# Performance work log

Hardware: AMD Instinct MI355X
Metric: run time of the kernel (lower is better)

The kernel has to match this reference:

```python
import jax, jax.numpy as jnp
import numpy as np

G = 16          # groups
K = 5           # kernel_size
IPG = 1024 // G # in_channels_per_group
OPG = 1024 // G # out_channels_per_group


def setup_inputs() -> dict:
    key = jax.random.key(0)
    k1, k2, k3 = jax.random.split(key, 3)
    inputs = jax.random.normal(k1, (4, 4096, 1024), dtype=jnp.float32)
    positions = jnp.sort(
        jax.random.randint(k2, (4, 4096), 0, 8192, dtype=jnp.int32), axis=-1)
    # kaiming-uniform-like init for kernel [G, OPG, IPG, K]
    fan_in = IPG * K
    bound = float(np.sqrt(6.0 / fan_in))
    kernel = jax.random.uniform(k3, (G, OPG, IPG, K), dtype=jnp.float32,
                                minval=-bound, maxval=bound)
    return {"inputs": inputs, "positions": positions, "kernel": kernel}


def reference(inputs, positions, kernel):
    B, L, C = inputs.shape
    c = K // 2
    # pad sequence dim; pad positions with -1 sentinel (never matches expected)
    pi = jnp.pad(inputs, ((0, 0), (c, c), (0, 0)))            # [B, L+2c, C]
    pp = jnp.pad(positions, ((0, 0), (c, c)), constant_values=-1)  # [B, L+2c]
    # sliding-window gather indices (equivalent to unfold with stride 1)
    idx = jnp.arange(L)[:, None] + jnp.arange(K)[None, :]      # [L, K]
    ip = pi[:, idx, :]        # [B, L, K, C] input patches
    ppatch = pp[:, idx]       # [B, L, K]  position patches
    # center of each patch is the original position at that output index
    offsets = jnp.arange(-c, c + 1, dtype=positions.dtype)    # [K]
    expected = positions[:, :, None] + offsets                # [B, L, K]
    mask = (ppatch == expected).astype(inputs.dtype)          # [B, L, K]
    masked = ip * mask[..., None]                             # [B, L, K, C]
    # split channels into groups: [B, L, K, G, IPG]
    gp = masked.reshape(B, L, K, G, IPG)
    # grouped conv reduce over in_channels_per_group and kernel taps
    out = jnp.einsum('blkgi,goik->blgo', gp, kernel)           # [B, L, G, OPG]
    return out
```

## Files before the change

kernel.cpp:

```cpp
#include <hip/hip_runtime.h>

typedef __attribute__((ext_vector_type(8))) short short8;
typedef __attribute__((ext_vector_type(4))) float float4v;
typedef __attribute__((ext_vector_type(4))) unsigned short us4;

namespace {
constexpr int NG   = 16;
constexpr int LSEQ = 4096;
constexpr int CIN  = 1024;
constexpr int IPG  = 64;
constexpr int OPG  = 64;
constexpr int KT   = 5;
constexpr int ROWS = 128;
constexpr int SIN_STRIDE = 72;
constexpr int SIN_ROWS   = ROWS + KT - 1;
constexpr int KSTEPS = 10;
constexpr size_t WFRAG_SHORTS = (size_t)NG * 4 * KSTEPS * 512;
constexpr size_t WFRAG_BYTES  = WFRAG_SHORTS * 2;
}

__device__ __forceinline__ unsigned short f2bf(float f) {
  unsigned int u = __builtin_bit_cast(unsigned int, f);
  u += 0x7fffu + ((u >> 16) & 1u);
  return (unsigned short)(u >> 16);
}

__global__ __launch_bounds__(256) void wprep(const float* __restrict__ gwt,
                                             unsigned short* __restrict__ wfrag) {
  const int u = blockIdx.x * 256 + threadIdx.x;
  const int E    = u * 8;
  const int tile = E >> 9;
  const int w9   = E & 511;
  const int n    = w9 >> 5;
  const int quad = (w9 & 31) >> 3;
  const int ks   = tile % KSTEPS;
  const int tt   = tile / KSTEPS;
  const int t    = tt & 3;
  const int g    = tt >> 2;
  const int tap  = ks >> 1;
  const int h    = ks & 1;
  const int o    = t * 16 + n;
  const float* src = gwt + (((size_t)(g * 64 + o) * 64) + h * 32 + quad * 8) * KT + tap;
  short8 v;
  #pragma unroll
  for (int j = 0; j < 8; ++j)
    v[j] = (short)f2bf(src[j * KT]);
  *(short8*)(wfrag + E) = v;
}

__global__ __launch_bounds__(256, 4) void mconv_main(
    const float* __restrict__ gin,
    const int* __restrict__ gpos,
    const unsigned short* __restrict__ wfrag,
    float* __restrict__ gout) {
  __shared__ __align__(16) unsigned short sIn[SIN_ROWS * SIN_STRIDE];
  __shared__ unsigned char sMaskB[ROWS];

  const int tid  = threadIdx.x;
  const int wv   = tid >> 6;
  const int lane = tid & 63;
  const int quad = lane >> 4;
  const int l16  = lane & 15;
  const int wm   = wv & 1;
  const int wn   = wv >> 1;

  const int g  = blockIdx.y;
  const int b  = blockIdx.z;
  const int l0 = blockIdx.x * ROWS;
  const int bL = b * LSEQ;

  for (int u = tid; u < SIN_ROWS * 16; u += 256) {
    const int r  = u >> 4;
    const int c4 = u & 15;
    const int l  = l0 - 2 + r;
    us4 w = {0, 0, 0, 0};
    if (l >= 0 && l < LSEQ) {
      float4v v = *(const float4v*)(gin + (size_t)(bL + l) * CIN + g * IPG + c4 * 4);
      w[0] = f2bf(v[0]); w[1] = f2bf(v[1]); w[2] = f2bf(v[2]); w[3] = f2bf(v[3]);
    }
    const int p = (c4 * 4 + ((r & 3) << 4)) & 63;
    *(us4*)(&sIn[r * SIN_STRIDE + p]) = w;
  }

  if (tid < ROWS) {
    const int l = l0 + tid;
    const int pc = gpos[bL + l];
    unsigned int mbits = 0;
    #pragma unroll
    for (int tap = 0; tap < KT; ++tap) {
      const int lsrc = l + tap - 2;
      int ok = 0;
      if (lsrc >= 0 && lsrc < LSEQ)
        ok = (gpos[bL + lsrc] == pc + (tap - 2));
      mbits |= (unsigned int)ok << tap;
    }
    sMaskB[tid] = (unsigned char)mbits;
  }
  __syncthreads();

  int mb[4];
  #pragma unroll
  for (int mt = 0; mt < 4; ++mt)
    mb[mt] = sMaskB[wm * 64 + mt * 16 + l16];

  const int laneoff = l16 * 32 + quad * 8;
  const unsigned short* wb0 = wfrag + (size_t)((g * 4 + wn * 2) * KSTEPS) * 512 + laneoff;
  const unsigned short* wb1 = wb0 + (size_t)KSTEPS * 512;

  const short8 zero8 = {0, 0, 0, 0, 0, 0, 0, 0};
  const float4v zf = {0.f, 0.f, 0.f, 0.f};
  float4v acc[4][2];
  #pragma unroll
  for (int mt = 0; mt < 4; ++mt) { acc[mt][0] = zf; acc[mt][1] = zf; }

  short8 bc0 = *(const short8*)(wb0);
  short8 bc1 = *(const short8*)(wb1);

  #pragma unroll 2
  for (int ks = 0; ks < KSTEPS; ++ks) {
    const int ksn = (ks + 1 < KSTEPS) ? ks + 1 : KSTEPS - 1;
    short8 bn0 = *(const short8*)(wb0 + ksn * 512);
    short8 bn1 = *(const short8*)(wb1 + ksn * 512);
    const int tap = ks >> 1;
    const int h   = ks & 1;
    const int s   = h * 32 + quad * 8;
    #pragma unroll
    for (int mt = 0; mt < 4; ++mt) {
      const int r  = wm * 64 + mt * 16 + l16 + tap;
      const int sp = (s + ((r & 3) << 4)) & 63;
      short8 a = *(const short8*)(&sIn[r * SIN_STRIDE + sp]);
      if (!((mb[mt] >> tap) & 1)) a = zero8;
      acc[mt][0] = __builtin_amdgcn_mfma_f32_16x16x32_bf16(a, bc0, acc[mt][0], 0, 0, 0);
      acc[mt][1] = __builtin_amdgcn_mfma_f32_16x16x32_bf16(a, bc1, acc[mt][1], 0, 0, 0);
    }
    bc0 = bn0; bc1 = bn1;
  }

  #pragma unroll
  for (int mt = 0; mt < 4; ++mt) {
    const int lrow = l0 + wm * 64 + mt * 16 + quad * 4;
    #pragma unroll
    for (int reg = 0; reg < 4; ++reg) {
      float* orow = gout + (size_t)(bL + lrow + reg) * CIN + g * OPG + wn * 32;
      orow[l16]      = acc[mt][0][reg];
      orow[16 + l16] = acc[mt][1][reg];
    }
  }
}

namespace fb {
constexpr int ROWS_PER_CHUNK = 128;
constexpr int CHUNKS = 4;
constexpr int ROWS_PER_BLOCK = 512;
constexpr int SW_STRIDE  = 328;
constexpr int FSIN_STRIDE = 72;
constexpr int FSIN_ROWS   = 132;
}

__global__ __launch_bounds__(256, 2) void mconv_f32_mfma(
    const float* __restrict__ gin, const int* __restrict__ gpos,
    const float* __restrict__ gwt, float* __restrict__ gout) {
  using namespace fb;
  __shared__ __align__(16) unsigned short sW[OPG * SW_STRIDE];
  __shared__ __align__(16) unsigned short sIn[FSIN_ROWS * FSIN_STRIDE];
  __shared__ unsigned char sMask[ROWS_PER_CHUNK * KT];

  const int tid  = threadIdx.x;
  const int wave = tid >> 6;
  const int lane = tid & 63;
  const int quad = lane >> 4;
  const int l16  = lane & 15;
  const int g  = blockIdx.y;
  const int b  = blockIdx.z;
  const int tile0 = blockIdx.x * ROWS_PER_BLOCK;
  const int bL = b * LSEQ;

  {
    const float* wg = gwt + (size_t)g * (OPG * IPG * KT);
    for (int u = tid; u < (OPG * IPG * KT) / 4; u += 256) {
      const int base = u * 4;
      float4v v = *(const float4v*)(wg + base);
      int o = base / (IPG * KT);
      int r = base - o * (IPG * KT);
      int i = r / KT;
      int k = r - i * KT;
      int addr = o * SW_STRIDE + k * IPG + i;
      #pragma unroll
      for (int t = 0; t < 4; ++t) {
        sW[addr] = f2bf(v[t]);
        ++k; addr += IPG;
        if (k == KT) { k = 0; ++i; addr -= KT * IPG - 1; }
      }
    }
  }
  const short8 zero8 = {0,0,0,0,0,0,0,0};
  const float4v zf = {0.f,0.f,0.f,0.f};
  for (int ch = 0; ch < CHUNKS; ++ch) {
    const int l0 = tile0 + ch * ROWS_PER_CHUNK;
    __syncthreads();
    for (int t = tid; t < ROWS_PER_CHUNK * KT; t += 256) {
      const int lr = t / KT, tap = t - lr * KT, l = l0 + lr, lsrc = l + tap - 2;
      int ok = 0;
      if (lsrc >= 0 && lsrc < LSEQ) ok = (gpos[bL + lsrc] == gpos[bL + l] + (tap - 2));
      sMask[t] = (unsigned char)ok;
    }
    for (int u = tid; u < FSIN_ROWS * 16; u += 256) {
      const int r = u >> 4, c4 = u & 15, l = l0 - 2 + r;
      us4 w = {0,0,0,0};
      if (l >= 0 && l < LSEQ) {
        float4v v = *(const float4v*)(gin + (size_t)(bL + l) * CIN + g * IPG + c4 * 4);
        w[0]=f2bf(v[0]); w[1]=f2bf(v[1]); w[2]=f2bf(v[2]); w[3]=f2bf(v[3]);
      }
      *(us4*)(&sIn[r * FSIN_STRIDE + c4 * 4]) = w;
    }
    __syncthreads();
    float4v acc[2][4];
    #pragma unroll
    for (int mm = 0; mm < 2; ++mm)
      #pragma unroll
      for (int nt = 0; nt < 4; ++nt) acc[mm][nt] = zf;
    const int m0 = wave * 32 + l16, m1 = m0 + 16;
    #pragma unroll
    for (int tap = 0; tap < KT; ++tap) {
      const bool msk0 = sMask[m0 * KT + tap] != 0;
      const bool msk1 = sMask[m1 * KT + tap] != 0;
      #pragma unroll
      for (int h = 0; h < 2; ++h) {
        const int kk = tap * IPG + h * 32 + quad * 8;
        const short8 b0 = *(const short8*)(&sW[(0*16 + l16) * SW_STRIDE + kk]);
        const short8 b1 = *(const short8*)(&sW[(1*16 + l16) * SW_STRIDE + kk]);
        const short8 b2 = *(const short8*)(&sW[(2*16 + l16) * SW_STRIDE + kk]);
        const short8 b3 = *(const short8*)(&sW[(3*16 + l16) * SW_STRIDE + kk]);
        const int ci = h * 32 + quad * 8;
        short8 a0 = *(const short8*)(&sIn[(m0 + tap) * FSIN_STRIDE + ci]);
        short8 a1 = *(const short8*)(&sIn[(m1 + tap) * FSIN_STRIDE + ci]);
        if (!msk0) a0 = zero8;
        if (!msk1) a1 = zero8;
        acc[0][0] = __builtin_amdgcn_mfma_f32_16x16x32_bf16(a0,b0,acc[0][0],0,0,0);
        acc[0][1] = __builtin_amdgcn_mfma_f32_16x16x32_bf16(a0,b1,acc[0][1],0,0,0);
        acc[0][2] = __builtin_amdgcn_mfma_f32_16x16x32_bf16(a0,b2,acc[0][2],0,0,0);
        acc[0][3] = __builtin_amdgcn_mfma_f32_16x16x32_bf16(a0,b3,acc[0][3],0,0,0);
        acc[1][0] = __builtin_amdgcn_mfma_f32_16x16x32_bf16(a1,b0,acc[1][0],0,0,0);
        acc[1][1] = __builtin_amdgcn_mfma_f32_16x16x32_bf16(a1,b1,acc[1][1],0,0,0);
        acc[1][2] = __builtin_amdgcn_mfma_f32_16x16x32_bf16(a1,b2,acc[1][2],0,0,0);
        acc[1][3] = __builtin_amdgcn_mfma_f32_16x16x32_bf16(a1,b3,acc[1][3],0,0,0);
      }
    }
    #pragma unroll
    for (int mm = 0; mm < 2; ++mm) {
      const int lrow = l0 + wave * 32 + mm * 16 + quad * 4;
      #pragma unroll
      for (int reg = 0; reg < 4; ++reg) {
        float* orow = gout + ((size_t)(bL + lrow + reg) * NG + g) * OPG;
        #pragma unroll
        for (int nt = 0; nt < 4; ++nt)
          orow[nt * 16 + l16] = acc[mm][nt][reg];
      }
    }
  }
}

extern "C" void kernel_launch(void* const* d_in, const int* in_sizes, int n_in,
                              void* d_out, int out_size, void* d_ws, size_t ws_size,
                              hipStream_t stream) {
  (void)in_sizes; (void)n_in; (void)out_size;
  const float* gin  = (const float*)d_in[0];
  const int*   gpos = (const int*)d_in[1];
  const float* gwt  = (const float*)d_in[2];
  float*       gout = (float*)d_out;

  if (ws_size >= WFRAG_BYTES) {
    unsigned short* wfrag = (unsigned short*)d_ws;
    hipLaunchKernelGGL(wprep, dim3(160), dim3(256), 0, stream, gwt, wfrag);
    dim3 grid(LSEQ / ROWS, NG, 4);
    hipLaunchKernelGGL(mconv_main, grid, dim3(256), 0, stream,
                       gin, gpos, wfrag, gout);
  } else {
    dim3 grid(LSEQ / fb::ROWS_PER_BLOCK, NG, 4);
    hipLaunchKernelGGL(mconv_f32_mfma, grid, dim3(256), 0, stream,
                       gin, gpos, gwt, gout);
  }
}
```

Before: 132.4 us.

## Stream input fragments directly from global memory, dropping LDS staging

The main conv kernel no longer stages the bf16-converted input tile and mask in shared memory. Each wave owns a 32-row strip and all 64 output channels, and loads its A fragments per tap straight from global memory, converting to bf16 in registers. Masks are computed per lane with clamped indices. This removes the LDS fill, the block barrier and the shared-memory footprint. In exchange each input row is reloaded from global memory (or cache) five times, once per tap, and the fp32-to-bf16 conversion is repeated for each reload.

```diff
diff --git a/kernel.cpp b/kernel.cpp
--- a/kernel.cpp
+++ b/kernel.cpp
@@ -11,9 +11,6 @@
 constexpr int IPG  = 64;
 constexpr int OPG  = 64;
 constexpr int KT   = 5;
-constexpr int ROWS = 128;
-constexpr int SIN_STRIDE = 72;
-constexpr int SIN_ROWS   = ROWS + KT - 1;
 constexpr int KSTEPS = 10;
 constexpr size_t WFRAG_SHORTS = (size_t)NG * 4 * KSTEPS * 512;
 constexpr size_t WFRAG_BYTES  = WFRAG_SHORTS * 2;
@@ -23,6 +20,19 @@
   unsigned int u = __builtin_bit_cast(unsigned int, f);
   u += 0x7fffu + ((u >> 16) & 1u);
   return (unsigned short)(u >> 16);
+}
+
+__device__ __forceinline__ short8 cvt8(float4v v0, float4v v1) {
+  short8 r;
+  r[0] = (short)f2bf(v0[0]);
+  r[1] = (short)f2bf(v0[1]);
+  r[2] = (short)f2bf(v0[2]);
+  r[3] = (short)f2bf(v0[3]);
+  r[4] = (short)f2bf(v1[0]);
+  r[5] = (short)f2bf(v1[1]);
+  r[6] = (short)f2bf(v1[2]);
+  r[7] = (short)f2bf(v1[3]);
+  return r;
 }
 
 __global__ __launch_bounds__(256) void wprep(const float* __restrict__ gwt,
@@ -48,102 +58,91 @@
   *(short8*)(wfrag + E) = v;
 }
 
-__global__ __launch_bounds__(256, 4) void mconv_main(
+__global__ __launch_bounds__(256, 4) void mconv_stream(
     const float* __restrict__ gin,
     const int* __restrict__ gpos,
     const unsigned short* __restrict__ wfrag,
     float* __restrict__ gout) {
-  __shared__ __align__(16) unsigned short sIn[SIN_ROWS * SIN_STRIDE];
-  __shared__ unsigned char sMaskB[ROWS];
-
   const int tid  = threadIdx.x;
   const int wv   = tid >> 6;
   const int lane = tid & 63;
   const int quad = lane >> 4;
   const int l16  = lane & 15;
-  const int wm   = wv & 1;
-  const int wn   = wv >> 1;
 
   const int g  = blockIdx.y;
   const int b  = blockIdx.z;
-  const int l0 = blockIdx.x * ROWS;
+  const int strip0 = blockIdx.x * 128 + wv * 32;
   const int bL = b * LSEQ;
 
-  for (int u = tid; u < SIN_ROWS * 16; u += 256) {
-    const int r  = u >> 4;
-    const int c4 = u & 15;
-    const int l  = l0 - 2 + r;
-    us4 w = {0, 0, 0, 0};
-    if (l >= 0 && l < LSEQ) {
-      float4v v = *(const float4v*)(gin + (size_t)(bL + l) * CIN + g * IPG + c4 * 4);
-      w[0] = f2bf(v[0]); w[1] = f2bf(v[1]); w[2] = f2bf(v[2]); w[3] = f2bf(v[3]);
-    }
-    const int p = (c4 * 4 + ((r & 3) << 4)) & 63;
-    *(us4*)(&sIn[r * SIN_STRIDE + p]) = w;
-  }
-
-  if (tid < ROWS) {
-    const int l = l0 + tid;
+  int mb[2];
+  #pragma unroll
+  for (int mt = 0; mt < 2; ++mt) {
+    const int l  = strip0 + mt * 16 + l16;
     const int pc = gpos[bL + l];
-    unsigned int mbits = 0;
+    unsigned int bits = 0;
     #pragma unroll
     for (int tap = 0; tap < KT; ++tap) {
       const int lsrc = l + tap - 2;
-      int ok = 0;
-      if (lsrc >= 0 && lsrc < LSEQ)
-        ok = (gpos[bL + lsrc] == pc + (tap - 2));
-      mbits |= (unsigned int)ok << tap;
-    }
-    sMaskB[tid] = (unsigned char)mbits;
-  }
-  __syncthreads();
-
-  int mb[4];
-  #pragma unroll
-  for (int mt = 0; mt < 4; ++mt)
-    mb[mt] = sMaskB[wm * 64 + mt * 16 + l16];
-
-  const int laneoff = l16 * 32 + quad * 8;
-  const unsigned short* wb0 = wfrag + (size_t)((g * 4 + wn * 2) * KSTEPS) * 512 + laneoff;
-  const unsigned short* wb1 = wb0 + (size_t)KSTEPS * 512;
+      const int lc   = min(max(lsrc, 0), LSEQ - 1);
+      const int ok   = (lsrc == lc) & (gpos[bL + lc] == pc + (tap - 2));
+      bits |= (unsigned int)ok << tap;
+    }
+    mb[mt] = (int)bits;
+  }
+
+  const unsigned short* wbase = wfrag + (size_t)(g * 4) * KSTEPS * 512
+                                      + l16 * 32 + quad * 8;
 
   const short8 zero8 = {0, 0, 0, 0, 0, 0, 0, 0};
   const float4v zf = {0.f, 0.f, 0.f, 0.f};
-  float4v acc[4][2];
-  #pragma unroll
-  for (int mt = 0; mt < 4; ++mt) { acc[mt][0] = zf; acc[mt][1] = zf; }
-
-  short8 bc0 = *(const short8*)(wb0);
-  short8 bc1 = *(const short8*)(wb1);
-
-  #pragma unroll 2
-  for (int ks = 0; ks < KSTEPS; ++ks) {
-    const int ksn = (ks + 1 < KSTEPS) ? ks + 1 : KSTEPS - 1;
-    short8 bn0 = *(const short8*)(wb0 + ksn * 512);
-    short8 bn1 = *(const short8*)(wb1 + ksn * 512);
-    const int tap = ks >> 1;
-    const int h   = ks & 1;
-    const int s   = h * 32 + quad * 8;
-    #pragma unroll
-    for (int mt = 0; mt < 4; ++mt) {
-      const int r  = wm * 64 + mt * 16 + l16 + tap;
-      const int sp = (s + ((r & 3) << 4)) & 63;
-      short8 a = *(const short8*)(&sIn[r * SIN_STRIDE + sp]);
-      if (!((mb[mt] >> tap) & 1)) a = zero8;
-      acc[mt][0] = __builtin_amdgcn_mfma_f32_16x16x32_bf16(a, bc0, acc[mt][0], 0, 0, 0);
-      acc[mt][1] = __builtin_amdgcn_mfma_f32_16x16x32_bf16(a, bc1, acc[mt][1], 0, 0, 0);
-    }
-    bc0 = bn0; bc1 = bn1;
-  }
-
-  #pragma unroll
-  for (int mt = 0; mt < 4; ++mt) {
-    const int lrow = l0 + wm * 64 + mt * 16 + quad * 4;
+  float4v acc[2][4];
+  #pragma unroll
+  for (int mt = 0; mt < 2; ++mt)
+    #pragma unroll
+    for (int nt = 0; nt < 4; ++nt)
+      acc[mt][nt] = zf;
+
+  const float* ginb = gin + (size_t)bL * CIN + g * IPG + quad * 8;
+
+  #pragma unroll
+  for (int tap = 0; tap < KT; ++tap) {
+    short8 afr[2][2];
+    #pragma unroll
+    for (int mt = 0; mt < 2; ++mt) {
+      const int lsrc = strip0 + mt * 16 + l16 + tap - 2;
+      const int lc   = min(max(lsrc, 0), LSEQ - 1);
+      const float* rp = ginb + (size_t)lc * CIN;
+      const bool ok = (mb[mt] >> tap) & 1;
+      #pragma unroll
+      for (int h = 0; h < 2; ++h) {
+        float4v v0 = *(const float4v*)(rp + h * 32);
+        float4v v1 = *(const float4v*)(rp + h * 32 + 4);
+        short8 a = cvt8(v0, v1);
+        if (!ok) a = zero8;
+        afr[mt][h] = a;
+      }
+    }
+    #pragma unroll
+    for (int h = 0; h < 2; ++h) {
+      const int ks = tap * 2 + h;
+      #pragma unroll
+      for (int nt = 0; nt < 4; ++nt) {
+        const short8 bfr = *(const short8*)(wbase + (size_t)(nt * KSTEPS + ks) * 512);
+        acc[0][nt] = __builtin_amdgcn_mfma_f32_16x16x32_bf16(afr[0][h], bfr, acc[0][nt], 0, 0, 0);
+        acc[1][nt] = __builtin_amdgcn_mfma_f32_16x16x32_bf16(afr[1][h], bfr, acc[1][nt], 0, 0, 0);
+      }
+    }
+  }
+
+  #pragma unroll
+  for (int mt = 0; mt < 2; ++mt) {
+    const int lrow = strip0 + mt * 16 + quad * 4;
     #pragma unroll
     for (int reg = 0; reg < 4; ++reg) {
-      float* orow = gout + (size_t)(bL + lrow + reg) * CIN + g * OPG + wn * 32;
-      orow[l16]      = acc[mt][0][reg];
-      orow[16 + l16] = acc[mt][1][reg];
+      float* orow = gout + (size_t)(bL + lrow + reg) * CIN + g * OPG;
+      #pragma unroll
+      for (int nt = 0; nt < 4; ++nt)
+        orow[nt * 16 + l16] = acc[mt][nt][reg];
     }
   }
 }
@@ -272,8 +271,8 @@
   if (ws_size >= WFRAG_BYTES) {
     unsigned short* wfrag = (unsigned short*)d_ws;
     hipLaunchKernelGGL(wprep, dim3(160), dim3(256), 0, stream, gwt, wfrag);
-    dim3 grid(LSEQ / ROWS, NG, 4);
-    hipLaunchKernelGGL(mconv_main, grid, dim3(256), 0, stream,
+    dim3 grid(LSEQ / 128, NG, 4);
+    hipLaunchKernelGGL(mconv_stream, grid, dim3(256), 0, stream,
                        gin, gpos, wfrag, gout);
   } else {
     dim3 grid(LSEQ / fb::ROWS_PER_BLOCK, NG, 4);
```

After: 161.3 us. 1.22x slower.
